# Optimization experiments

Measured on AMD Instinct MI355X. Metric: run time of the kernel, lower is better.

The kernel has to match this reference:

```python
import jax, jax.numpy as jnp
import numpy as np

B = 16384
SIZES = [512, 256, 256, 128]  # layer_sizes, layer 0 = clamped input
K = 16        # settling iterations
ETA = 0.1     # eta_x, scale 'none' => effective eta per layer = 0.1
CLIP = 1.0    # dx_clip


def setup_inputs() -> dict:
    key = jax.random.key(0)
    k0, k1, k2, k3 = jax.random.split(key, 4)
    x0 = jax.random.normal(k0, (B, SIZES[0]), jnp.float32)
    # W[l]: (D_{l+1}, D_l), init scale 1/sqrt(D_{l+1}) as in torch code
    W0 = jax.random.normal(k1, (SIZES[1], SIZES[0]), jnp.float32) * (1.0 / np.sqrt(SIZES[1]))
    W1 = jax.random.normal(k2, (SIZES[2], SIZES[1]), jnp.float32) * (1.0 / np.sqrt(SIZES[2]))
    W2 = jax.random.normal(k3, (SIZES[3], SIZES[2]), jnp.float32) * (1.0 / np.sqrt(SIZES[3]))
    return {"x0": x0, "W0": W0, "W1": W1, "W2": W2}


def _f(z):
    return jnp.tanh(z)


def _f_prime(z):
    t = jnp.tanh(z)
    return 1.0 - t * t


def _settle(x0, Ws):
    """Run K settling steps. Layer 0 clamped to x0; layers 1..L free."""
    L = len(Ws)
    bsz = x0.shape[0]
    xs0 = (x0,) + tuple(jnp.zeros((bsz, w.shape[0]), x0.dtype) for w in Ws)

    def step(xs, _):
        xs = list(xs)
        # top-down predictions: preact[l] = x[l+1] @ W[l], shape (B, D_l)
        preacts = [xs[l + 1] @ Ws[l] for l in range(L)]
        errs = [xs[l] - _f(preacts[l]) for l in range(L)]
        new = [xs[0]]  # layer 0 clamped
        for l in range(1, L + 1):
            # feedback: (e[l-1] * f'(preact[l-1])) @ W[l-1].T  (tied weights)
            dx = (errs[l - 1] * _f_prime(preacts[l - 1])) @ Ws[l - 1].T
            if l < L:
                dx = dx - errs[l]
            dx = jnp.clip(dx, -CLIP, CLIP)
            new.append(xs[l] + ETA * dx)
        return tuple(new), None

    final, _ = jax.lax.scan(step, xs0, None, length=K)
    return final


def reference(x0, W0, W1, W2):
    final = _settle(x0, (W0, W1, W2))
    # return settled latent (layer L) state, shape (B, 128)
    return final[-1]
```

## Files before the change

### kernel.cpp

```cpp
#include <hip/hip_runtime.h>

typedef _Float16 half8 __attribute__((ext_vector_type(8)));
typedef float floatx4 __attribute__((ext_vector_type(4)));

#define DEV_INLINE __device__ __forceinline__

constexpr int D0 = 512, D1 = 256, D2 = 256, D3 = 128;
constexpr int NROWS = 16384;
constexpr int MBLK = 32;
constexpr int NBLK = NROWS / MBLK;
constexpr int KITERS = 16;
constexpr float ETA = 0.1f;

constexpr int OFF_WF0 = 0;
constexpr int OFF_WF1 = OFF_WF0 + D1 * D0;
constexpr int OFF_WF2 = OFF_WF1 + D2 * D1;
constexpr int OFF_WB0 = OFF_WF2 + D3 * D2;
constexpr int OFF_WB1 = OFF_WB0 + D0 * D1;
constexpr int OFF_WB2 = OFF_WB1 + D1 * D2;
constexpr int PACK_ELEMS = OFF_WB2 + D2 * D3;

__global__ void repack_kernel(const float* __restrict__ W0, const float* __restrict__ W1,
                              const float* __restrict__ W2, _Float16* __restrict__ pack) {
  int p = blockIdx.x * 256 + threadIdx.x;
  if (p >= PACK_ELEMS) return;
  const float* W; int Csrc, Nd, off; bool tr;
  if (p < OFF_WF1)      { W = W0; Csrc = D0; Nd = D0; off = OFF_WF0; tr = false; }
  else if (p < OFF_WF2) { W = W1; Csrc = D1; Nd = D1; off = OFF_WF1; tr = false; }
  else if (p < OFF_WB0) { W = W2; Csrc = D2; Nd = D2; off = OFF_WF2; tr = false; }
  else if (p < OFF_WB1) { W = W0; Csrc = D0; Nd = D1; off = OFF_WB0; tr = true;  }
  else if (p < OFF_WB2) { W = W1; Csrc = D1; Nd = D1; off = OFF_WB1; tr = true;  }
  else                  { W = W2; Csrc = D2; Nd = D3; off = OFF_WB2; tr = true;  }
  int local = p - off;
  int j  = local & 7;
  int l  = (local >> 3) & 63;
  int fr = local >> 9;
  int NT = Nd >> 4;
  int nt = fr % NT, kt = fr / NT;
  int k = kt * 32 + ((l >> 4) << 3) + j;
  int n = nt * 16 + (l & 15);
  float v = tr ? W[n * Csrc + k] : W[k * Csrc + n];
  pack[p] = (_Float16)v;
}

DEV_INLINE float fast_tanh(float x) {
  float e = __expf(2.f * x);
  return 1.f - 2.f * __builtin_amdgcn_rcpf(e + 1.f);
}

DEV_INLINE const _Float16* bpt(const _Float16* Bp, int nt, int lane) {
  return Bp + ((size_t)nt * 64 + lane) * 8;
}

template <int RT, int KSTEPS, int NTT, int STRB, int ASd>
DEV_INLINE void mm_reg(const char* __restrict__ A, const _Float16* __restrict__ bsrc,
                       int lane, floatx4* acc) {
  const int arow = lane & 15;
  const int aoff = (lane >> 4) << 4;
  half8 bq[KSTEPS];
#pragma unroll
  for (int s = 0; s < KSTEPS; ++s)
    bq[s] = *(const half8*)(bsrc + (size_t)s * NTT * 512);
#pragma unroll
  for (int k0 = 0; k0 < KSTEPS; ++k0) {
    half8 a[RT];
#pragma unroll
    for (int rt = 0; rt < RT; ++rt) {
      int row = rt * 16 + arow;
      int byte = (row * STRB + k0 * 64 + aoff) ^ ((row & 7) << 4);
      a[rt] = *(const half8*)(A + byte);
    }
#pragma unroll
    for (int rt = 0; rt < RT; ++rt)
      acc[rt * ASd] =
          __builtin_amdgcn_mfma_f32_16x16x32_f16(a[rt], bq[k0], acc[rt * ASd], 0, 0, 0);
  }
}

__global__ __launch_bounds__(512)
void settle_kernel(const float* __restrict__ x0,
                   const _Float16* __restrict__ pack,
                   float* __restrict__ out) {
  extern __shared__ char lds[];
  char* AX1 = lds;
  char* AG0 = lds + 16384;
  char* AQ  = lds + 24576;
  char* AG1 = lds + 40960;
  char* AR  = lds + 57344;

  const int tid  = threadIdx.x;
  const int lane = tid & 63;
  const int wave = tid >> 6;
  const int row0 = blockIdx.x * MBLK;
  const int rsub = (lane >> 4) << 2;
  const int csub = lane & 15;

  half8 x0r[4];
#pragma unroll
  for (int q = 0; q < 4; ++q)
#pragma unroll
    for (int rt = 0; rt < 2; ++rt)
#pragma unroll
      for (int i = 0; i < 4; ++i) {
        int row = rt * 16 + rsub + i;
        int col = (q * 8 + wave) * 16 + csub;
        float v = x0[(size_t)(row0 + row) * D0 + col];
        int li = (q * 2 + rt) * 4 + i;
        x0r[li >> 3][li & 7] = (_Float16)v;
      }

  {
    floatx4 z = {0.f, 0.f, 0.f, 0.f};
    for (int i = tid; i < 1024; i += 512) ((floatx4*)AQ)[i] = z;
    for (int i = tid; i < 512; i += 512) ((floatx4*)AR)[i] = z;
  }

  const floatx4 zf = {0.f, 0.f, 0.f, 0.f};
  floatx4 x3m[2];
#pragma unroll
  for (int i = 0; i < 2; ++i) x3m[i] = zf;

  const _Float16* Wf0 = pack + OFF_WF0;
  const _Float16* Wf1 = pack + OFF_WF1;
  const _Float16* Wf2 = pack + OFF_WF2;
  const _Float16* Wb0 = pack + OFF_WB0;
  const _Float16* Wb1 = pack + OFF_WB1;
  const _Float16* Wb2 = pack + OFF_WB2;

  {
    floatx4 dx1a[4];
#pragma unroll
    for (int i = 0; i < 4; ++i) dx1a[i] = zf;
    for (int q = 0; q < 4; ++q) {
#pragma unroll
      for (int rt = 0; rt < 2; ++rt)
#pragma unroll
        for (int i = 0; i < 4; ++i) {
          int row = rt * 16 + rsub + i;
          int colq = wave * 16 + csub;
          int li = (q * 2 + rt) * 4 + i;
          int byte = (row * 256 + colq * 2) ^ ((row & 7) << 4);
          *(_Float16*)(AG0 + byte) = x0r[li >> 3][li & 7];
        }
      __syncthreads();
#pragma unroll
      for (int ct = 0; ct < 2; ++ct)
        mm_reg<2, 4, 16, 256, 2>(AG0, bpt(Wb0 + q * 32768, wave * 2 + ct, lane), lane,
                                 &dx1a[ct]);
      __syncthreads();
    }
#pragma unroll
    for (int rt = 0; rt < 2; ++rt)
#pragma unroll
      for (int ct = 0; ct < 2; ++ct) {
        int col = (wave * 2 + ct) * 16 + csub;
#pragma unroll
        for (int i = 0; i < 4; ++i) {
          int row = rt * 16 + rsub + i;
          float dx = fminf(1.f, fmaxf(-1.f, dx1a[rt * 2 + ct][i]));
          int byte = (row * 512 + col * 2) ^ ((row & 7) << 4);
          *(_Float16*)(AX1 + byte) = (_Float16)(ETA * dx);
        }
      }
    __syncthreads();
  }

  for (int it = 1; it < KITERS; ++it) {
    floatx4 dx1a[4];
    {
#pragma unroll
      for (int i = 0; i < 4; ++i) dx1a[i] = zf;
#pragma unroll
      for (int ct = 0; ct < 2; ++ct)
        mm_reg<2, 8, 16, 512, 2>(AQ, bpt(Wf1, wave * 2 + ct, lane), lane, &dx1a[ct]);
#pragma unroll
      for (int rt = 0; rt < 2; ++rt)
#pragma unroll
        for (int ct = 0; ct < 2; ++ct) {
          int col = (wave * 2 + ct) * 16 + csub;
#pragma unroll
          for (int i = 0; i < 4; ++i) {
            int row = rt * 16 + rsub + i;
            int sb = (row * 512 + col * 2) ^ ((row & 7) << 4);
            float t = fast_tanh(dx1a[rt * 2 + ct][i]);
            float x1o = (float)*(const _Float16*)(AX1 + sb);
            float e = x1o - t;
            *(_Float16*)(AG1 + sb) = (_Float16)(e * (1.f - t * t));
            dx1a[rt * 2 + ct][i] = -e;
          }
        }
    }
    for (int q = 0; q < 4; ++q) {
      {
        floatx4 acc3[2];
#pragma unroll
        for (int i = 0; i < 2; ++i) acc3[i] = zf;
        mm_reg<2, 8, 32, 512, 1>(AX1, bpt(Wf0, q * 8 + wave, lane), lane, acc3);
        int colq = wave * 16 + csub;
#pragma unroll
        for (int rt = 0; rt < 2; ++rt)
#pragma unroll
          for (int i = 0; i < 4; ++i) {
            int row = rt * 16 + rsub + i;
            int li = (q * 2 + rt) * 4 + i;
            float t = fast_tanh(acc3[rt][i]);
            float xv = (float)x0r[li >> 3][li & 7];
            float g = (xv - t) * (1.f - t * t);
            int byte = (row * 256 + colq * 2) ^ ((row & 7) << 4);
            *(_Float16*)(AG0 + byte) = (_Float16)g;
          }
      }
      __syncthreads();
#pragma unroll
      for (int ct = 0; ct < 2; ++ct)
        mm_reg<2, 4, 16, 256, 2>(AG0, bpt(Wb0 + q * 32768, wave * 2 + ct, lane), lane,
                                 &dx1a[ct]);
      __syncthreads();
    }
#pragma unroll
    for (int rt = 0; rt < 2; ++rt)
#pragma unroll
      for (int ct = 0; ct < 2; ++ct) {
        int col = (wave * 2 + ct) * 16 + csub;
#pragma unroll
        for (int i = 0; i < 4; ++i) {
          int row = rt * 16 + rsub + i;
          int sb = (row * 512 + col * 2) ^ ((row & 7) << 4);
          float dx = fminf(1.f, fmaxf(-1.f, dx1a[rt * 2 + ct][i]));
          float x1o = (float)*(const _Float16*)(AX1 + sb);
          *(_Float16*)(AX1 + sb) = (_Float16)(x1o + ETA * dx);
        }
      }
    floatx4 dx2a[4];
    half8 g2h[2];
    {
      floatx4 p2[4];
#pragma unroll
      for (int i = 0; i < 4; ++i) p2[i] = zf;
#pragma unroll
      for (int ct = 0; ct < 2; ++ct)
        mm_reg<2, 4, 16, 256, 2>(AR, bpt(Wf2, wave * 2 + ct, lane), lane, &p2[ct]);
#pragma unroll
      for (int rt = 0; rt < 2; ++rt)
#pragma unroll
        for (int ct = 0; ct < 2; ++ct) {
          int col = (wave * 2 + ct) * 16 + csub;
#pragma unroll
          for (int i = 0; i < 4; ++i) {
            int row = rt * 16 + rsub + i;
            int sb = (row * 512 + col * 2) ^ ((row & 7) << 4);
            float t = fast_tanh(p2[rt * 2 + ct][i]);
            float x2o = (float)*(const _Float16*)(AQ + sb);
            float e = x2o - t;
            int li = (rt * 2 + ct) * 4 + i;
            g2h[li >> 3][li & 7] = (_Float16)(e * (1.f - t * t));
            dx2a[rt * 2 + ct][i] = -e;
          }
        }
    }
    {
#pragma unroll
      for (int ct = 0; ct < 2; ++ct)
        mm_reg<2, 8, 16, 512, 2>(AG1, bpt(Wb1, wave * 2 + ct, lane), lane, &dx2a[ct]);
#pragma unroll
      for (int rt = 0; rt < 2; ++rt)
#pragma unroll
        for (int ct = 0; ct < 2; ++ct) {
          int col = (wave * 2 + ct) * 16 + csub;
#pragma unroll
          for (int i = 0; i < 4; ++i) {
            int row = rt * 16 + rsub + i;
            int sb = (row * 512 + col * 2) ^ ((row & 7) << 4);
            float dx = fminf(1.f, fmaxf(-1.f, dx2a[rt * 2 + ct][i]));
            float x2o = (float)*(const _Float16*)(AQ + sb);
            *(_Float16*)(AQ + sb) = (_Float16)(x2o + ETA * dx);
          }
        }
    }
    __syncthreads();
#pragma unroll
    for (int rt = 0; rt < 2; ++rt)
#pragma unroll
      for (int ct = 0; ct < 2; ++ct) {
        int col = (wave * 2 + ct) * 16 + csub;
#pragma unroll
        for (int i = 0; i < 4; ++i) {
          int row = rt * 16 + rsub + i;
          int sb = (row * 512 + col * 2) ^ ((row & 7) << 4);
          int li = (rt * 2 + ct) * 4 + i;
          *(_Float16*)(AG1 + sb) = g2h[li >> 3][li & 7];
        }
      }
    __syncthreads();
    {
      floatx4 acc6[2];
#pragma unroll
      for (int i = 0; i < 2; ++i) acc6[i] = zf;
      mm_reg<2, 8, 8, 512, 1>(AG1, bpt(Wb2, wave, lane), lane, acc6);
      __syncthreads();
      int col = wave * 16 + csub;
#pragma unroll
      for (int rt = 0; rt < 2; ++rt)
#pragma unroll
        for (int i = 0; i < 4; ++i) {
          int row = rt * 16 + rsub + i;
          float dx = fminf(1.f, fmaxf(-1.f, acc6[rt][i]));
          float nv = x3m[rt][i] + ETA * dx;
          x3m[rt][i] = nv;
          int byte = (row * 256 + col * 2) ^ ((row & 7) << 4);
          *(_Float16*)(AR + byte) = (_Float16)nv;
        }
    }
  }

  {
    int col = wave * 16 + csub;
#pragma unroll
    for (int rt = 0; rt < 2; ++rt)
#pragma unroll
      for (int i = 0; i < 4; ++i) {
        int row = rt * 16 + rsub + i;
        out[(size_t)(row0 + row) * D3 + col] = x3m[rt][i];
      }
  }
}

extern "C" void kernel_launch(void* const* d_in, const int* in_sizes, int n_in,
                              void* d_out, int out_size, void* d_ws, size_t ws_size,
                              hipStream_t stream) {
  const float* x0 = (const float*)d_in[0];
  const float* W0 = (const float*)d_in[1];
  const float* W1 = (const float*)d_in[2];
  const float* W2 = (const float*)d_in[3];
  float* out = (float*)d_out;

  _Float16* pack = (_Float16*)d_ws;
  repack_kernel<<<(PACK_ELEMS + 255) / 256, 256, 0, stream>>>(W0, W1, W2, pack);

  (void)hipFuncSetAttribute(reinterpret_cast<const void*>(settle_kernel),
                            hipFuncAttributeMaxDynamicSharedMemorySize, 65536);
  settle_kernel<<<NBLK, 512, 65536, stream>>>(x0, pack, out);
}
```

Before: 1.188 ms.

## Stream fp16 x0 from global instead of registers; batch two column tiles per GEMM

```diff
diff --git a/kernel.cpp b/kernel.cpp
--- a/kernel.cpp
+++ b/kernel.cpp
@@ -21,26 +21,32 @@
 constexpr int PACK_ELEMS = OFF_WB2 + D2 * D3;
 
 __global__ void repack_kernel(const float* __restrict__ W0, const float* __restrict__ W1,
-                              const float* __restrict__ W2, _Float16* __restrict__ pack) {
+                              const float* __restrict__ W2, const float* __restrict__ x0,
+                              _Float16* __restrict__ pack, _Float16* __restrict__ x0h,
+                              int do_x0) {
   int p = blockIdx.x * 256 + threadIdx.x;
-  if (p >= PACK_ELEMS) return;
-  const float* W; int Csrc, Nd, off; bool tr;
-  if (p < OFF_WF1)      { W = W0; Csrc = D0; Nd = D0; off = OFF_WF0; tr = false; }
-  else if (p < OFF_WF2) { W = W1; Csrc = D1; Nd = D1; off = OFF_WF1; tr = false; }
-  else if (p < OFF_WB0) { W = W2; Csrc = D2; Nd = D2; off = OFF_WF2; tr = false; }
-  else if (p < OFF_WB1) { W = W0; Csrc = D0; Nd = D1; off = OFF_WB0; tr = true;  }
-  else if (p < OFF_WB2) { W = W1; Csrc = D1; Nd = D1; off = OFF_WB1; tr = true;  }
-  else                  { W = W2; Csrc = D2; Nd = D3; off = OFF_WB2; tr = true;  }
-  int local = p - off;
-  int j  = local & 7;
-  int l  = (local >> 3) & 63;
-  int fr = local >> 9;
-  int NT = Nd >> 4;
-  int nt = fr % NT, kt = fr / NT;
-  int k = kt * 32 + ((l >> 4) << 3) + j;
-  int n = nt * 16 + (l & 15);
-  float v = tr ? W[n * Csrc + k] : W[k * Csrc + n];
-  pack[p] = (_Float16)v;
+  if (p < PACK_ELEMS) {
+    const float* W; int Csrc, Nd, off; bool tr;
+    if (p < OFF_WF1)      { W = W0; Csrc = D0; Nd = D0; off = OFF_WF0; tr = false; }
+    else if (p < OFF_WF2) { W = W1; Csrc = D1; Nd = D1; off = OFF_WF1; tr = false; }
+    else if (p < OFF_WB0) { W = W2; Csrc = D2; Nd = D2; off = OFF_WF2; tr = false; }
+    else if (p < OFF_WB1) { W = W0; Csrc = D0; Nd = D1; off = OFF_WB0; tr = true;  }
+    else if (p < OFF_WB2) { W = W1; Csrc = D1; Nd = D1; off = OFF_WB1; tr = true;  }
+    else                  { W = W2; Csrc = D2; Nd = D3; off = OFF_WB2; tr = true;  }
+    int local = p - off;
+    int j  = local & 7;
+    int l  = (local >> 3) & 63;
+    int fr = local >> 9;
+    int NT = Nd >> 4;
+    int nt = fr % NT, kt = fr / NT;
+    int k = kt * 32 + ((l >> 4) << 3) + j;
+    int n = nt * 16 + (l & 15);
+    float v = tr ? W[n * Csrc + k] : W[k * Csrc + n];
+    pack[p] = (_Float16)v;
+  } else if (do_x0) {
+    int q = p - PACK_ELEMS;
+    if (q < NROWS * D0) x0h[q] = (_Float16)x0[q];
+  }
 }
 
 DEV_INLINE float fast_tanh(float x) {
@@ -52,15 +58,18 @@
   return Bp + ((size_t)nt * 64 + lane) * 8;
 }
 
-template <int RT, int KSTEPS, int NTT, int STRB, int ASd>
-DEV_INLINE void mm_reg(const char* __restrict__ A, const _Float16* __restrict__ bsrc,
-                       int lane, floatx4* acc) {
+template <int RT, int KSTEPS, int CT, int NTT, int STRB, int AS>
+DEV_INLINE void mm_burst(const char* __restrict__ A, const _Float16* __restrict__ bsrc,
+                         int lane, floatx4* acc) {
+  static_assert(KSTEPS * CT <= 8, "bq register budget");
   const int arow = lane & 15;
   const int aoff = (lane >> 4) << 4;
-  half8 bq[KSTEPS];
+  half8 bq[KSTEPS * CT];
 #pragma unroll
   for (int s = 0; s < KSTEPS; ++s)
-    bq[s] = *(const half8*)(bsrc + (size_t)s * NTT * 512);
+#pragma unroll
+    for (int ct = 0; ct < CT; ++ct)
+      bq[s * CT + ct] = *(const half8*)(bsrc + (size_t)(s * NTT + ct) * 512);
 #pragma unroll
   for (int k0 = 0; k0 < KSTEPS; ++k0) {
     half8 a[RT];
@@ -71,14 +80,17 @@
       a[rt] = *(const half8*)(A + byte);
     }
 #pragma unroll
-    for (int rt = 0; rt < RT; ++rt)
-      acc[rt * ASd] =
-          __builtin_amdgcn_mfma_f32_16x16x32_f16(a[rt], bq[k0], acc[rt * ASd], 0, 0, 0);
+    for (int ct = 0; ct < CT; ++ct)
+#pragma unroll
+      for (int rt = 0; rt < RT; ++rt)
+        acc[rt * AS + ct] =
+            __builtin_amdgcn_mfma_f32_16x16x32_f16(a[rt], bq[k0 * CT + ct], acc[rt * AS + ct], 0, 0, 0);
   }
 }
 
 __global__ __launch_bounds__(512)
 void settle_kernel(const float* __restrict__ x0,
+                   const _Float16* __restrict__ x0h,
                    const _Float16* __restrict__ pack,
                    float* __restrict__ out) {
   extern __shared__ char lds[];
@@ -95,20 +107,6 @@
   const int rsub = (lane >> 4) << 2;
   const int csub = lane & 15;
 
-  half8 x0r[4];
-#pragma unroll
-  for (int q = 0; q < 4; ++q)
-#pragma unroll
-    for (int rt = 0; rt < 2; ++rt)
-#pragma unroll
-      for (int i = 0; i < 4; ++i) {
-        int row = rt * 16 + rsub + i;
-        int col = (q * 8 + wave) * 16 + csub;
-        float v = x0[(size_t)(row0 + row) * D0 + col];
-        int li = (q * 2 + rt) * 4 + i;
-        x0r[li >> 3][li & 7] = (_Float16)v;
-      }
-
   {
     floatx4 z = {0.f, 0.f, 0.f, 0.f};
     for (int i = tid; i < 1024; i += 512) ((floatx4*)AQ)[i] = z;
@@ -132,21 +130,15 @@
 #pragma unroll
     for (int i = 0; i < 4; ++i) dx1a[i] = zf;
     for (int q = 0; q < 4; ++q) {
-#pragma unroll
-      for (int rt = 0; rt < 2; ++rt)
-#pragma unroll
-        for (int i = 0; i < 4; ++i) {
-          int row = rt * 16 + rsub + i;
-          int colq = wave * 16 + csub;
-          int li = (q * 2 + rt) * 4 + i;
-          int byte = (row * 256 + colq * 2) ^ ((row & 7) << 4);
-          *(_Float16*)(AG0 + byte) = x0r[li >> 3][li & 7];
-        }
-      __syncthreads();
-#pragma unroll
-      for (int ct = 0; ct < 2; ++ct)
-        mm_reg<2, 4, 16, 256, 2>(AG0, bpt(Wb0 + q * 32768, wave * 2 + ct, lane), lane,
-                                 &dx1a[ct]);
+      for (int idx = tid; idx < MBLK * 128; idx += 512) {
+        int row = idx >> 7, colq = idx & 127;
+        size_t gi = (size_t)(row0 + row) * D0 + q * 128 + colq;
+        _Float16 v = x0h ? x0h[gi] : (_Float16)x0[gi];
+        int byte = (row * 256 + colq * 2) ^ ((row & 7) << 4);
+        *(_Float16*)(AG0 + byte) = v;
+      }
+      __syncthreads();
+      mm_burst<2, 4, 2, 16, 256, 2>(AG0, bpt(Wb0 + q * 32768, wave * 2, lane), lane, dx1a);
       __syncthreads();
     }
 #pragma unroll
@@ -172,7 +164,7 @@
       for (int i = 0; i < 4; ++i) dx1a[i] = zf;
 #pragma unroll
       for (int ct = 0; ct < 2; ++ct)
-        mm_reg<2, 8, 16, 512, 2>(AQ, bpt(Wf1, wave * 2 + ct, lane), lane, &dx1a[ct]);
+        mm_burst<2, 8, 1, 16, 512, 2>(AQ, bpt(Wf1, wave * 2 + ct, lane), lane, &dx1a[ct]);
 #pragma unroll
       for (int rt = 0; rt < 2; ++rt)
 #pragma unroll
@@ -195,26 +187,23 @@
         floatx4 acc3[2];
 #pragma unroll
         for (int i = 0; i < 2; ++i) acc3[i] = zf;
-        mm_reg<2, 8, 32, 512, 1>(AX1, bpt(Wf0, q * 8 + wave, lane), lane, acc3);
+        mm_burst<2, 8, 1, 32, 512, 1>(AX1, bpt(Wf0, q * 8 + wave, lane), lane, acc3);
         int colq = wave * 16 + csub;
 #pragma unroll
         for (int rt = 0; rt < 2; ++rt)
 #pragma unroll
           for (int i = 0; i < 4; ++i) {
             int row = rt * 16 + rsub + i;
-            int li = (q * 2 + rt) * 4 + i;
             float t = fast_tanh(acc3[rt][i]);
-            float xv = (float)x0r[li >> 3][li & 7];
+            size_t gi = (size_t)(row0 + row) * D0 + q * 128 + colq;
+            float xv = x0h ? (float)x0h[gi] : x0[gi];
             float g = (xv - t) * (1.f - t * t);
             int byte = (row * 256 + colq * 2) ^ ((row & 7) << 4);
             *(_Float16*)(AG0 + byte) = (_Float16)g;
           }
       }
       __syncthreads();
-#pragma unroll
-      for (int ct = 0; ct < 2; ++ct)
-        mm_reg<2, 4, 16, 256, 2>(AG0, bpt(Wb0 + q * 32768, wave * 2 + ct, lane), lane,
-                                 &dx1a[ct]);
+      mm_burst<2, 4, 2, 16, 256, 2>(AG0, bpt(Wb0 + q * 32768, wave * 2, lane), lane, dx1a);
       __syncthreads();
     }
 #pragma unroll
@@ -237,9 +226,7 @@
       floatx4 p2[4];
 #pragma unroll
       for (int i = 0; i < 4; ++i) p2[i] = zf;
-#pragma unroll
-      for (int ct = 0; ct < 2; ++ct)
-        mm_reg<2, 4, 16, 256, 2>(AR, bpt(Wf2, wave * 2 + ct, lane), lane, &p2[ct]);
+      mm_burst<2, 4, 2, 16, 256, 2>(AR, bpt(Wf2, wave * 2, lane), lane, p2);
 #pragma unroll
       for (int rt = 0; rt < 2; ++rt)
 #pragma unroll
@@ -261,7 +248,7 @@
     {
 #pragma unroll
       for (int ct = 0; ct < 2; ++ct)
-        mm_reg<2, 8, 16, 512, 2>(AG1, bpt(Wb1, wave * 2 + ct, lane), lane, &dx2a[ct]);
+        mm_burst<2, 8, 1, 16, 512, 2>(AG1, bpt(Wb1, wave * 2 + ct, lane), lane, &dx2a[ct]);
 #pragma unroll
       for (int rt = 0; rt < 2; ++rt)
 #pragma unroll
@@ -296,7 +283,7 @@
       floatx4 acc6[2];
 #pragma unroll
       for (int i = 0; i < 2; ++i) acc6[i] = zf;
-      mm_reg<2, 8, 8, 512, 1>(AG1, bpt(Wb2, wave, lane), lane, acc6);
+      mm_burst<2, 8, 1, 8, 512, 1>(AG1, bpt(Wb2, wave, lane), lane, acc6);
       __syncthreads();
       int col = wave * 16 + csub;
 #pragma unroll
@@ -335,9 +322,15 @@
   float* out = (float*)d_out;
 
   _Float16* pack = (_Float16*)d_ws;
-  repack_kernel<<<(PACK_ELEMS + 255) / 256, 256, 0, stream>>>(W0, W1, W2, pack);
+  const size_t pack_bytes = (size_t)PACK_ELEMS * 2;
+  const size_t x0h_bytes = (size_t)NROWS * D0 * 2;
+  int do_x0 = (ws_size >= pack_bytes + x0h_bytes) ? 1 : 0;
+  _Float16* x0h = do_x0 ? (_Float16*)((char*)d_ws + pack_bytes) : nullptr;
+
+  int total = PACK_ELEMS + (do_x0 ? NROWS * D0 : 0);
+  repack_kernel<<<(total + 255) / 256, 256, 0, stream>>>(W0, W1, W2, x0, pack, x0h, do_x0);
 
   (void)hipFuncSetAttribute(reinterpret_cast<const void*>(settle_kernel),
                             hipFuncAttributeMaxDynamicSharedMemorySize, 65536);
-  settle_kernel<<<NBLK, 512, 65536, stream>>>(x0, pack, out);
-}
+  settle_kernel<<<NBLK, 512, 65536, stream>>>(x0, x0h, pack, out);
+}
```

Result: faster. 991.3 us, median of 2 (-16.6%).
